# Kernel tuning notes

Hardware: AMD Instinct MI355X
Metric: run time of the kernel (lower is better)

The kernel has to match this reference:

```python
import jax, jax.numpy as jnp
import numpy as np

N_NODES = 100000
IN_CH = 256
OUT_CH = 128
HID = 2 * OUT_CH  # 256
N_EDGES = 1600000


def gcn_conv(x, src, dst, W, b, num_nodes):
    """PyG GCNConv: add self-loops, symmetric deg^-1/2 normalization,
    linear transform, scatter-add aggregation, plus bias."""
    h = x @ W  # [N, F_out]
    loop = jnp.arange(num_nodes, dtype=src.dtype)
    src_f = jnp.concatenate([src, loop])
    dst_f = jnp.concatenate([dst, loop])
    ones = jnp.ones(src_f.shape[0], dtype=h.dtype)
    deg = jax.ops.segment_sum(ones, dst_f, num_segments=num_nodes)
    dis = jnp.where(deg > 0, jax.lax.rsqrt(deg), 0.0)
    norm = dis[src_f] * dis[dst_f]  # [E+N]
    msg = h[src_f] * norm[:, None]  # [E+N, F_out]
    out = jax.ops.segment_sum(msg, dst_f, num_segments=num_nodes)
    return out + b


def setup_inputs() -> dict:
    key = jax.random.key(0)
    ks = jax.random.split(key, 8)
    x = jax.random.normal(ks[0], (N_NODES, IN_CH), dtype=jnp.float32)
    edge_index = jax.random.randint(ks[1], (2, N_EDGES), 0, N_NODES, dtype=jnp.int64 if jax.config.jax_enable_x64 else jnp.int32)
    s1 = 1.0 / np.sqrt(IN_CH)
    s2 = 1.0 / np.sqrt(HID)
    W1 = jax.random.uniform(ks[2], (IN_CH, HID), jnp.float32, -s1, s1)
    b1 = jnp.zeros((HID,), jnp.float32)
    W_mu = jax.random.uniform(ks[3], (HID, OUT_CH), jnp.float32, -s2, s2)
    b_mu = jnp.zeros((OUT_CH,), jnp.float32)
    W_lv = jax.random.uniform(ks[4], (HID, OUT_CH), jnp.float32, -s2, s2)
    b_lv = jnp.zeros((OUT_CH,), jnp.float32)
    return {"x": x, "edge_index": edge_index, "W1": W1, "b1": b1,
            "W_mu": W_mu, "b_mu": b_mu, "W_lv": W_lv, "b_lv": b_lv}


def reference(x, edge_index, W1, b1, W_mu, b_mu, W_lv, b_lv):
    src, dst = edge_index[0], edge_index[1]
    h = jax.nn.relu(gcn_conv(x, src, dst, W1, b1, N_NODES))
    mu = gcn_conv(h, src, dst, W_mu, b_mu, N_NODES)
    logvar = gcn_conv(h, src, dst, W_lv, b_lv, N_NODES)
    return (mu, logvar)
```

## Files before the change

kernel.cpp:

```cpp
#include <hip/hip_runtime.h>
#include <hip/hip_fp16.h>

#define N_NODES 100000
#define E_EDGES 1600000
#define F 256
#define LV_OFF 12800000
#define NBUK 782
#define EPB 8192
#define NBLK_BIN 196

typedef _Float16 half8 __attribute__((ext_vector_type(8)));
typedef _Float16 f16x4 __attribute__((ext_vector_type(4)));
typedef float    f32x4 __attribute__((ext_vector_type(4)));

__global__ void k_zero(int* __restrict__ p, int n) {
    int i = blockIdx.x * 256 + threadIdx.x;
    if (i < n) p[i] = 0;
}

__global__ __launch_bounds__(256) void k_wprep_binA(
    const float* __restrict__ W1, const float* __restrict__ Wmu, const float* __restrict__ Wlv,
    _Float16* __restrict__ Wt1, _Float16* __restrict__ Wtc,
    const int* __restrict__ dst, int* __restrict__ gcnt, int* __restrict__ cbase)
{
    __shared__ int h[NBUK];
    int bid = blockIdx.x, tid = threadIdx.x;
    if (bid < 256) {
        int idx = bid * 256 + tid;
        int n = idx >> 8, k = idx & 255;
        Wt1[n * 256 + k] = (_Float16)W1[k * 256 + n];
        float wc = (n < 128) ? Wmu[k * 128 + n] : Wlv[k * 128 + (n - 128)];
        Wtc[n * 256 + k] = (_Float16)wc;
        return;
    }
    int blk = bid - 256;
    for (int b = tid; b < NBUK; b += 256) h[b] = 0;
    __syncthreads();
    int e0 = blk * EPB, e1 = min(e0 + EPB, E_EDGES);
    for (int e = e0 + tid; e < e1; e += 256) atomicAdd(&h[dst[e] >> 7], 1);
    __syncthreads();
    for (int b = tid; b < NBUK; b += 256) {
        int c = h[b];
        cbase[blk * NBUK + b] = c ? atomicAdd(&gcnt[b], c) : 0;
    }
}

__global__ __launch_bounds__(1024) void k_scan782(const int* __restrict__ gcnt,
                                                  int* __restrict__ gbase) {
    __shared__ int sd[1024];
    int tid = threadIdx.x;
    int v = (tid < NBUK) ? gcnt[tid] : 0;
    sd[tid] = v;
    __syncthreads();
    for (int off = 1; off < 1024; off <<= 1) {
        int t = (tid >= off) ? sd[tid - off] : 0;
        __syncthreads();
        sd[tid] += t;
        __syncthreads();
    }
    if (tid < NBUK) gbase[tid] = sd[tid] - v;
    if (tid == NBUK - 1) gbase[NBUK] = sd[tid];
}

__global__ __launch_bounds__(256) void k_binD(const unsigned long long* __restrict__ ebuf,
                                              const int* __restrict__ gbase,
                                              int* __restrict__ csr_src, int* __restrict__ row_off,
                                              float* __restrict__ dis) {
    __shared__ int dh[128], dsc[128], dcur[128];
    int b = blockIdx.x, tid = threadIdx.x;
    if (tid < 128) dh[tid] = 0;
    __syncthreads();
    int s0 = gbase[b], s1 = gbase[b + 1];
    for (int i = s0 + tid; i < s1; i += 256)
        atomicAdd(&dh[(int)(ebuf[i] >> 32) & 127], 1);
    __syncthreads();
    if (tid < 128) dsc[tid] = dh[tid];
    __syncthreads();
    for (int off = 1; off < 128; off <<= 1) {
        int t = 0;
        if (tid < 128 && tid >= off) t = dsc[tid - off];
        __syncthreads();
        if (tid < 128) dsc[tid] += t;
        __syncthreads();
    }
    if (tid < 128) {
        int ex = dsc[tid] - dh[tid];
        dcur[tid] = ex;
        int node = b * 128 + tid;
        if (node < N_NODES) {
            row_off[node] = s0 + ex;
            dis[node] = rsqrtf((float)dh[tid] + 1.0f);
        }
    }
    if (b == 0 && tid == 128) row_off[N_NODES] = E_EDGES;
    __syncthreads();
    for (int i = s0 + tid; i < s1; i += 256) {
        unsigned long long ed = ebuf[i];
        int dl = (int)(ed >> 32) & 127;
        int lr = atomicAdd(&dcur[dl], 1);
        csr_src[s0 + lr] = (int)(ed & 0xFFFFFFFFull);
    }
}

template <typename TA>
__device__ __forceinline__ void gemm_tile(
    const TA* __restrict__ A, const _Float16* __restrict__ Bt,
    _Float16* __restrict__ G, int M, int m0, int tid, _Float16* Ah, _Float16* Bh)
{
    const int wave = tid >> 6, lane = tid & 63;
    const int wm   = wave & 1, wn = wave >> 1;
    const int lrow = lane & 15, kgrp = lane >> 4;

    f32x4 acc[4][8];
#pragma unroll
    for (int i = 0; i < 4; i++)
#pragma unroll
        for (int j = 0; j < 8; j++) acc[i][j] = (f32x4){0.f, 0.f, 0.f, 0.f};

    for (int kt = 0; kt < 256; kt += 64) {
        if constexpr (sizeof(TA) == 4) {
            const int sr = tid >> 4, kq = tid & 15;
#pragma unroll
            for (int p = 0; p < 8; ++p) {
                int row = p * 16 + sr;
                int gm = m0 + row; if (gm >= M) gm = M - 1;
                float4 v = *reinterpret_cast<const float4*>((const float*)A + (size_t)gm * F + kt + kq * 4);
                f16x4 h4;
                h4[0] = (_Float16)v.x; h4[1] = (_Float16)v.y;
                h4[2] = (_Float16)v.z; h4[3] = (_Float16)v.w;
                *reinterpret_cast<f16x4*>(&Ah[row * 64 + ((kq * 4) ^ ((row & 7) << 3))]) = h4;
            }
        } else {
#pragma unroll
            for (int p = 0; p < 4; ++p) {
                int u = p * 256 + tid;
                int row = u >> 3, slot = u & 7;
                int gm = m0 + row; if (gm >= M) gm = M - 1;
                half8 v = *reinterpret_cast<const half8*>((const _Float16*)A + (size_t)gm * F + kt + slot * 8);
                *reinterpret_cast<half8*>(&Ah[row * 64 + ((slot * 8) ^ ((row & 7) << 3))]) = v;
            }
        }
#pragma unroll
        for (int p = 0; p < 8; ++p) {
            int u = p * 256 + tid;
            int n = u >> 3, slot = u & 7;
            half8 v = *reinterpret_cast<const half8*>(Bt + (size_t)n * F + kt + slot * 8);
            *reinterpret_cast<half8*>(&Bh[n * 64 + ((slot * 8) ^ ((n & 7) << 3))]) = v;
        }
        __syncthreads();
#pragma unroll
        for (int ks = 0; ks < 2; ++ks) {
            int kk = ks * 32 + kgrp * 8;
            half8 ah[4], bh[8];
#pragma unroll
            for (int i = 0; i < 4; ++i) {
                int row = wm * 64 + i * 16 + lrow;
                ah[i] = *reinterpret_cast<const half8*>(&Ah[row * 64 + (kk ^ ((row & 7) << 3))]);
            }
#pragma unroll
            for (int j = 0; j < 8; ++j) {
                int col = wn * 128 + j * 16 + lrow;
                bh[j] = *reinterpret_cast<const half8*>(&Bh[col * 64 + (kk ^ ((col & 7) << 3))]);
            }
#pragma unroll
            for (int i = 0; i < 4; ++i)
#pragma unroll
                for (int j = 0; j < 8; ++j)
                    acc[i][j] = __builtin_amdgcn_mfma_f32_16x16x32_f16(ah[i], bh[j], acc[i][j], 0, 0, 0);
        }
        __syncthreads();
    }

#pragma unroll
    for (int i = 0; i < 4; ++i) {
#pragma unroll
        for (int r = 0; r < 4; ++r) {
            int m = m0 + wm * 64 + i * 16 + kgrp * 4 + r;
            if (m >= M) continue;
#pragma unroll
            for (int j = 0; j < 8; ++j) {
                int n = wn * 128 + j * 16 + lrow;
                G[(size_t)m * F + n] = (_Float16)(acc[i][j][r]);
            }
        }
    }
}

__global__ __launch_bounds__(256, 2) void k_gemm_binC(
    const float* __restrict__ A, const _Float16* __restrict__ Bt,
    _Float16* __restrict__ G, int M,
    const int* __restrict__ src, const int* __restrict__ dst,
    const int* __restrict__ gbase, const int* __restrict__ cbase,
    unsigned long long* __restrict__ ebuf)
{
    __shared__ _Float16 smem[128 * 64 + 256 * 64];
    int bid = blockIdx.x, tid = threadIdx.x;
    int r5 = bid % 5;
    if (r5 < 4) {
        int gid = (bid / 5) * 4 + r5;
        if (gid < 782)
            gemm_tile<float>(A, Bt, G, M, gid * 128, tid, smem, smem + 128 * 64);
        return;
    }
    int* h2 = (int*)smem;
    int* bs = h2 + NBUK;
    int blk = bid / 5;
    for (int b = tid; b < NBUK; b += 256) {
        h2[b] = 0;
        bs[b] = gbase[b] + cbase[blk * NBUK + b];
    }
    __syncthreads();
    int e0 = blk * EPB, e1 = min(e0 + EPB, E_EDGES);
    for (int e = e0 + tid; e < e1; e += 256) {
        int d = dst[e];
        int b = d >> 7;
        int lr = atomicAdd(&h2[b], 1);
        ebuf[bs[b] + lr] = ((unsigned long long)(unsigned)d << 32) | (unsigned)src[e];
    }
}

__global__ __launch_bounds__(256, 2) void k_gemm_f16(
    const _Float16* __restrict__ A, const _Float16* __restrict__ Bt,
    _Float16* __restrict__ G, int M)
{
    __shared__ _Float16 smem[128 * 64 + 256 * 64];
    gemm_tile<_Float16>(A, Bt, G, M, blockIdx.x * 128, threadIdx.x, smem, smem + 128 * 64);
}

template <int RELU>
__device__ __forceinline__ void aggregate_body(
    const _Float16* __restrict__ g, const int* __restrict__ row_off,
    const int* __restrict__ csr_src, const float* __restrict__ dis,
    const float* __restrict__ bmu, const float* __restrict__ blv,
    _Float16* __restrict__ hout, float* __restrict__ out)
{
    int d = blockIdx.x * 4 + (threadIdx.x >> 6);
    int lane = threadIdx.x & 63;
    int hf = lane >> 5, lp = lane & 31;
    const half8* g8 = reinterpret_cast<const half8*>(g);
    float dd = dis[d];
    float a0[8] = {0,0,0,0,0,0,0,0}, a1[8] = {0,0,0,0,0,0,0,0};
    float a2[8] = {0,0,0,0,0,0,0,0}, a3[8] = {0,0,0,0,0,0,0,0};
    if (hf == 0) {
        half8 sv = g8[(size_t)d * 32 + lp];
#pragma unroll
        for (int k = 0; k < 8; k++) a0[k] = dd * (float)sv[k];
    }
    int j0 = row_off[d], j1 = row_off[d + 1];
    int j = j0 + hf;
    for (; j + 14 < j1; j += 16) {
        int s[8]; half8 v[8]; float dv[8];
#pragma unroll
        for (int p = 0; p < 8; ++p) s[p] = csr_src[j + 2 * p];
#pragma unroll
        for (int p = 0; p < 8; ++p) v[p] = g8[(size_t)s[p] * 32 + lp];
#pragma unroll
        for (int p = 0; p < 8; ++p) dv[p] = dis[s[p]];
#pragma unroll
        for (int k = 0; k < 8; k++) {
            a0[k] += dv[0] * (float)v[0][k]; a1[k] += dv[1] * (float)v[1][k];
            a2[k] += dv[2] * (float)v[2][k]; a3[k] += dv[3] * (float)v[3][k];
            a0[k] += dv[4] * (float)v[4][k]; a1[k] += dv[5] * (float)v[5][k];
            a2[k] += dv[6] * (float)v[6][k]; a3[k] += dv[7] * (float)v[7][k];
        }
    }
    for (; j + 2 < j1; j += 4) {
        int sA = csr_src[j], sB = csr_src[j + 2];
        half8 vA = g8[(size_t)sA * 32 + lp];
        half8 vB = g8[(size_t)sB * 32 + lp];
        float dA = dis[sA], dB = dis[sB];
#pragma unroll
        for (int k = 0; k < 8; k++) { a0[k] += dA * (float)vA[k]; a1[k] += dB * (float)vB[k]; }
    }
    if (j < j1) {
        int sA = csr_src[j];
        half8 vA = g8[(size_t)sA * 32 + lp];
        float dA = dis[sA];
#pragma unroll
        for (int k = 0; k < 8; k++) a0[k] += dA * (float)vA[k];
    }
#pragma unroll
    for (int k = 0; k < 8; k++) {
        a0[k] += a1[k] + a2[k] + a3[k];
        a0[k] += __shfl_xor(a0[k], 32);
    }
    if (RELU) {
        int c = lp * 8 + hf * 4;
        float4 bb = *reinterpret_cast<const float4*>(bmu + c);
        f16x4 o;
        o[0] = (_Float16)fmaxf(fmaf(dd, a0[hf * 4 + 0], bb.x), 0.0f);
        o[1] = (_Float16)fmaxf(fmaf(dd, a0[hf * 4 + 1], bb.y), 0.0f);
        o[2] = (_Float16)fmaxf(fmaf(dd, a0[hf * 4 + 2], bb.z), 0.0f);
        o[3] = (_Float16)fmaxf(fmaf(dd, a0[hf * 4 + 3], bb.w), 0.0f);
        *reinterpret_cast<f16x4*>(hout + (size_t)d * F + c) = o;
    } else {
        int ch = lp * 8 + hf * 4;
        float va = a0[hf * 4 + 0], vb = a0[hf * 4 + 1], vc = a0[hf * 4 + 2], vd = a0[hf * 4 + 3];
        if (ch < 128) {
            float4 bb = *reinterpret_cast<const float4*>(bmu + ch);
            float4 o = make_float4(fmaf(dd, va, bb.x), fmaf(dd, vb, bb.y),
                                   fmaf(dd, vc, bb.z), fmaf(dd, vd, bb.w));
            *reinterpret_cast<float4*>(out + (size_t)d * 128 + ch) = o;
        } else {
            int c2 = ch - 128;
            float4 bb = *reinterpret_cast<const float4*>(blv + c2);
            float4 o = make_float4(fmaf(dd, va, bb.x), fmaf(dd, vb, bb.y),
                                   fmaf(dd, vc, bb.z), fmaf(dd, vd, bb.w));
            *reinterpret_cast<float4*>(out + LV_OFF + (size_t)d * 128 + c2) = o;
        }
    }
}

__global__ __launch_bounds__(256) void k_aggregate_relu(
    const _Float16* __restrict__ g, const int* __restrict__ row_off,
    const int* __restrict__ csr_src, const float* __restrict__ dis,
    const float* __restrict__ b, _Float16* __restrict__ h)
{
    aggregate_body<1>(g, row_off, csr_src, dis, b, nullptr, h, nullptr);
}

__global__ __launch_bounds__(256) void k_aggregate_out(
    const _Float16* __restrict__ g, const int* __restrict__ row_off,
    const int* __restrict__ csr_src, const float* __restrict__ dis,
    const float* __restrict__ bmu, const float* __restrict__ blv,
    float* __restrict__ out)
{
    aggregate_body<0>(g, row_off, csr_src, dis, bmu, blv, nullptr, out);
}

extern "C" void kernel_launch(void* const* d_in, const int* in_sizes, int n_in,
                              void* d_out, int out_size, void* d_ws, size_t ws_size,
                              hipStream_t stream) {
    const float* x   = (const float*)d_in[0];
    const int*   ei  = (const int*)d_in[1];
    const int*   src = ei;
    const int*   dst = ei + E_EDGES;
    const float* W1  = (const float*)d_in[2];
    const float* b1  = (const float*)d_in[3];
    const float* Wmu = (const float*)d_in[4];
    const float* bmu = (const float*)d_in[5];
    const float* Wlv = (const float*)d_in[6];
    const float* blv = (const float*)d_in[7];
    float* out = (float*)d_out;

    char* ws = (char*)d_ws;
    size_t o = 0;
    auto carve = [&](size_t bytes) -> char* {
        char* p = ws + o;
        o = (o + bytes + 1023) & ~(size_t)1023;
        return p;
    };
    float*    dis     = (float*)   carve(400000);
    int*      row_off = (int*)     carve(400004);
    int*      gcnt    = (int*)     carve(NBUK * 4);
    int*      gbase   = (int*)     carve((NBUK + 1) * 4);
    int*      cbase   = (int*)     carve((size_t)NBLK_BIN * NBUK * 4);
    _Float16* Wt1     = (_Float16*)carve(131072);
    _Float16* Wtc     = (_Float16*)carve(131072);
    int*      csr_src = (int*)     carve((size_t)E_EDGES * 4);
    unsigned long long* ebuf = (unsigned long long*)carve((size_t)E_EDGES * 8);
    _Float16* g       = (_Float16*)carve((size_t)N_NODES * F * 2);
    (void)ws_size;

    _Float16* h16 = (_Float16*)(out + LV_OFF);

    k_zero      <<<(NBUK + 255) / 256, 256, 0, stream>>>(gcnt, NBUK);
    k_wprep_binA<<<256 + NBLK_BIN, 256, 0, stream>>>(W1, Wmu, Wlv, Wt1, Wtc, dst, gcnt, cbase);
    k_scan782   <<<1, 1024, 0, stream>>>(gcnt, gbase);
    k_gemm_binC <<<980, 256, 0, stream>>>(x, Wt1, g, N_NODES, src, dst, gbase, cbase, ebuf);
    k_binD      <<<NBUK, 256, 0, stream>>>(ebuf, gbase, csr_src, row_off, dis);

    k_aggregate_relu<<<N_NODES / 4, 256, 0, stream>>>(g, row_off, csr_src, dis, b1, h16);

    k_gemm_f16<<<782, 256, 0, stream>>>(h16, Wtc, g, N_NODES);
    k_aggregate_out<<<N_NODES / 4, 256, 0, stream>>>(g, row_off, csr_src, dis, bmu, blv, out);
}
```

Baseline: 422.7 us.

## Fold source-side degree scaling into GEMM epilogue and streamline aggregation

Per-node degree counts are now computed early with global atomics, so dis is available before the GEMMs. Each GEMM output row is pre-scaled by dis[src] in its epilogue. This removes the per-edge dis[s] gathers and multiplies from both aggregation kernels, whose inner loop becomes packed fp16-to-fp32 mix-FMAs (v_fma_mix_f32). The change also adds nontemporal loads for GEMM inputs and nontemporal output stores, and reduces the aggregation accumulators from four to two. The cost is an extra 1.6M-edge atomic count pass and an fp16 rounding of the pre-scaled values.

```diff
diff --git a/kernel.cpp b/kernel.cpp
--- a/kernel.cpp
+++ b/kernel.cpp
@@ -8,20 +8,38 @@
 #define NBUK 782
 #define EPB 8192
 #define NBLK_BIN 196
+#define CNT_BLKS 6250
 
 typedef _Float16 half8 __attribute__((ext_vector_type(8)));
 typedef _Float16 f16x4 __attribute__((ext_vector_type(4)));
 typedef float    f32x4 __attribute__((ext_vector_type(4)));
-
-__global__ void k_zero(int* __restrict__ p, int n) {
+typedef unsigned u32x4 __attribute__((ext_vector_type(4)));
+
+__device__ __forceinline__ void fmix2(float& lo, float& hi, unsigned v) {
+    asm("v_fma_mix_f32 %0, %2, 1.0, %0 op_sel_hi:[1,0,0]\n\t"
+        "v_fma_mix_f32 %1, %2, 1.0, %1 op_sel:[1,0,0] op_sel_hi:[1,0,0]"
+        : "+v"(lo), "+v"(hi) : "v"(v));
+}
+
+__device__ __forceinline__ void acc_row(float* a, half8 v) {
+    u32x4 u = __builtin_bit_cast(u32x4, v);
+    fmix2(a[0], a[1], u[0]);
+    fmix2(a[2], a[3], u[1]);
+    fmix2(a[4], a[5], u[2]);
+    fmix2(a[6], a[7], u[3]);
+}
+
+__global__ void k_zero2(int* __restrict__ cnt, int* __restrict__ gcnt) {
     int i = blockIdx.x * 256 + threadIdx.x;
-    if (i < n) p[i] = 0;
-}
-
-__global__ __launch_bounds__(256) void k_wprep_binA(
+    if (i < N_NODES) cnt[i] = 0;
+    if (i < NBUK) gcnt[i] = 0;
+}
+
+__global__ __launch_bounds__(256) void k_prep(
     const float* __restrict__ W1, const float* __restrict__ Wmu, const float* __restrict__ Wlv,
     _Float16* __restrict__ Wt1, _Float16* __restrict__ Wtc,
-    const int* __restrict__ dst, int* __restrict__ gcnt, int* __restrict__ cbase)
+    const int* __restrict__ dst, int* __restrict__ gcnt, int* __restrict__ cbase,
+    int* __restrict__ cnt)
 {
     __shared__ int h[NBUK];
     int bid = blockIdx.x, tid = threadIdx.x;
@@ -33,6 +51,11 @@
         Wtc[n * 256 + k] = (_Float16)wc;
         return;
     }
+    if (bid >= 256 + NBLK_BIN) {
+        int e = (bid - 256 - NBLK_BIN) * 256 + tid;
+        if (e < E_EDGES) atomicAdd(&cnt[dst[e]], 1);
+        return;
+    }
     int blk = bid - 256;
     for (int b = tid; b < NBUK; b += 256) h[b] = 0;
     __syncthreads();
@@ -45,10 +68,17 @@
     }
 }
 
-__global__ __launch_bounds__(1024) void k_scan782(const int* __restrict__ gcnt,
-                                                  int* __restrict__ gbase) {
+__global__ __launch_bounds__(1024) void k_scan_dis(const int* __restrict__ gcnt,
+                                                   int* __restrict__ gbase,
+                                                   const int* __restrict__ cnt,
+                                                   float* __restrict__ dis) {
+    int tid = threadIdx.x;
+    if (blockIdx.x != 0) {
+        int i = (blockIdx.x - 1) * 1024 + tid;
+        if (i < N_NODES) dis[i] = rsqrtf((float)cnt[i] + 1.0f);
+        return;
+    }
     __shared__ int sd[1024];
-    int tid = threadIdx.x;
     int v = (tid < NBUK) ? gcnt[tid] : 0;
     sd[tid] = v;
     __syncthreads();
@@ -64,8 +94,7 @@
 
 __global__ __launch_bounds__(256) void k_binD(const unsigned long long* __restrict__ ebuf,
                                               const int* __restrict__ gbase,
-                                              int* __restrict__ csr_src, int* __restrict__ row_off,
-                                              float* __restrict__ dis) {
+                                              int* __restrict__ csr_src, int* __restrict__ row_off) {
     __shared__ int dh[128], dsc[128], dcur[128];
     int b = blockIdx.x, tid = threadIdx.x;
     if (tid < 128) dh[tid] = 0;
@@ -87,10 +116,7 @@
         int ex = dsc[tid] - dh[tid];
         dcur[tid] = ex;
         int node = b * 128 + tid;
-        if (node < N_NODES) {
-            row_off[node] = s0 + ex;
-            dis[node] = rsqrtf((float)dh[tid] + 1.0f);
-        }
+        if (node < N_NODES) row_off[node] = s0 + ex;
     }
     if (b == 0 && tid == 128) row_off[N_NODES] = E_EDGES;
     __syncthreads();
@@ -105,7 +131,8 @@
 template <typename TA>
 __device__ __forceinline__ void gemm_tile(
     const TA* __restrict__ A, const _Float16* __restrict__ Bt,
-    _Float16* __restrict__ G, int M, int m0, int tid, _Float16* Ah, _Float16* Bh)
+    const float* __restrict__ dis, _Float16* __restrict__ G, int M,
+    int m0, int tid, _Float16* Ah, _Float16* Bh)
 {
     const int wave = tid >> 6, lane = tid & 63;
     const int wm   = wave & 1, wn = wave >> 1;
@@ -124,10 +151,11 @@
             for (int p = 0; p < 8; ++p) {
                 int row = p * 16 + sr;
                 int gm = m0 + row; if (gm >= M) gm = M - 1;
-                float4 v = *reinterpret_cast<const float4*>((const float*)A + (size_t)gm * F + kt + kq * 4);
+                f32x4 v = __builtin_nontemporal_load(
+                    reinterpret_cast<const f32x4*>((const float*)A + (size_t)gm * F + kt + kq * 4));
                 f16x4 h4;
-                h4[0] = (_Float16)v.x; h4[1] = (_Float16)v.y;
-                h4[2] = (_Float16)v.z; h4[3] = (_Float16)v.w;
+                h4[0] = (_Float16)v[0]; h4[1] = (_Float16)v[1];
+                h4[2] = (_Float16)v[2]; h4[3] = (_Float16)v[3];
                 *reinterpret_cast<f16x4*>(&Ah[row * 64 + ((kq * 4) ^ ((row & 7) << 3))]) = h4;
             }
         } else {
@@ -136,7 +164,8 @@
                 int u = p * 256 + tid;
                 int row = u >> 3, slot = u & 7;
                 int gm = m0 + row; if (gm >= M) gm = M - 1;
-                half8 v = *reinterpret_cast<const half8*>((const _Float16*)A + (size_t)gm * F + kt + slot * 8);
+                half8 v = __builtin_nontemporal_load(
+                    reinterpret_cast<const half8*>((const _Float16*)A + (size_t)gm * F + kt + slot * 8));
                 *reinterpret_cast<half8*>(&Ah[row * 64 + ((slot * 8) ^ ((row & 7) << 3))]) = v;
             }
         }
@@ -177,10 +206,11 @@
         for (int r = 0; r < 4; ++r) {
             int m = m0 + wm * 64 + i * 16 + kgrp * 4 + r;
             if (m >= M) continue;
+            float dv = dis[m];
 #pragma unroll
             for (int j = 0; j < 8; ++j) {
                 int n = wn * 128 + j * 16 + lrow;
-                G[(size_t)m * F + n] = (_Float16)(acc[i][j][r]);
+                G[(size_t)m * F + n] = (_Float16)(acc[i][j][r] * dv);
             }
         }
     }
@@ -188,7 +218,7 @@
 
 __global__ __launch_bounds__(256, 2) void k_gemm_binC(
     const float* __restrict__ A, const _Float16* __restrict__ Bt,
-    _Float16* __restrict__ G, int M,
+    const float* __restrict__ dis, _Float16* __restrict__ G, int M,
     const int* __restrict__ src, const int* __restrict__ dst,
     const int* __restrict__ gbase, const int* __restrict__ cbase,
     unsigned long long* __restrict__ ebuf)
@@ -199,7 +229,7 @@
     if (r5 < 4) {
         int gid = (bid / 5) * 4 + r5;
         if (gid < 782)
-            gemm_tile<float>(A, Bt, G, M, gid * 128, tid, smem, smem + 128 * 64);
+            gemm_tile<float>(A, Bt, dis, G, M, gid * 128, tid, smem, smem + 128 * 64);
         return;
     }
     int* h2 = (int*)smem;
@@ -221,10 +251,10 @@
 
 __global__ __launch_bounds__(256, 2) void k_gemm_f16(
     const _Float16* __restrict__ A, const _Float16* __restrict__ Bt,
-    _Float16* __restrict__ G, int M)
+    const float* __restrict__ dis, _Float16* __restrict__ G, int M)
 {
     __shared__ _Float16 smem[128 * 64 + 256 * 64];
-    gemm_tile<_Float16>(A, Bt, G, M, blockIdx.x * 128, threadIdx.x, smem, smem + 128 * 64);
+    gemm_tile<_Float16>(A, Bt, dis, G, M, blockIdx.x * 128, threadIdx.x, smem, smem + 128 * 64);
 }
 
 template <int RELU>
@@ -238,52 +268,44 @@
     int lane = threadIdx.x & 63;
     int hf = lane >> 5, lp = lane & 31;
     const half8* g8 = reinterpret_cast<const half8*>(g);
-    float dd = dis[d];
     float a0[8] = {0,0,0,0,0,0,0,0}, a1[8] = {0,0,0,0,0,0,0,0};
-    float a2[8] = {0,0,0,0,0,0,0,0}, a3[8] = {0,0,0,0,0,0,0,0};
     if (hf == 0) {
         half8 sv = g8[(size_t)d * 32 + lp];
 #pragma unroll
-        for (int k = 0; k < 8; k++) a0[k] = dd * (float)sv[k];
+        for (int k = 0; k < 8; k++) a0[k] = (float)sv[k];
     }
     int j0 = row_off[d], j1 = row_off[d + 1];
     int j = j0 + hf;
-    for (; j + 14 < j1; j += 16) {
-        int s[8]; half8 v[8]; float dv[8];
-#pragma unroll
-        for (int p = 0; p < 8; ++p) s[p] = csr_src[j + 2 * p];
-#pragma unroll
-        for (int p = 0; p < 8; ++p) v[p] = g8[(size_t)s[p] * 32 + lp];
-#pragma unroll
-        for (int p = 0; p < 8; ++p) dv[p] = dis[s[p]];
-#pragma unroll
-        for (int k = 0; k < 8; k++) {
-            a0[k] += dv[0] * (float)v[0][k]; a1[k] += dv[1] * (float)v[1][k];
-            a2[k] += dv[2] * (float)v[2][k]; a3[k] += dv[3] * (float)v[3][k];
-            a0[k] += dv[4] * (float)v[4][k]; a1[k] += dv[5] * (float)v[5][k];
-            a2[k] += dv[6] * (float)v[6][k]; a3[k] += dv[7] * (float)v[7][k];
-        }
+    for (; j + 10 < j1; j += 12) {
+        int s0 = csr_src[j],     s1 = csr_src[j + 2], s2 = csr_src[j + 4];
+        int s3 = csr_src[j + 6], s4 = csr_src[j + 8], s5 = csr_src[j + 10];
+        half8 v0 = g8[(size_t)s0 * 32 + lp];
+        half8 v1 = g8[(size_t)s1 * 32 + lp];
+        half8 v2 = g8[(size_t)s2 * 32 + lp];
+        half8 v3 = g8[(size_t)s3 * 32 + lp];
+        half8 v4 = g8[(size_t)s4 * 32 + lp];
+        half8 v5 = g8[(size_t)s5 * 32 + lp];
+        acc_row(a0, v0); acc_row(a1, v1);
+        acc_row(a0, v2); acc_row(a1, v3);
+        acc_row(a0, v4); acc_row(a1, v5);
     }
     for (; j + 2 < j1; j += 4) {
         int sA = csr_src[j], sB = csr_src[j + 2];
         half8 vA = g8[(size_t)sA * 32 + lp];
         half8 vB = g8[(size_t)sB * 32 + lp];
-        float dA = dis[sA], dB = dis[sB];
-#pragma unroll
-        for (int k = 0; k < 8; k++) { a0[k] += dA * (float)vA[k]; a1[k] += dB * (float)vB[k]; }
+        acc_row(a0, vA); acc_row(a1, vB);
     }
     if (j < j1) {
         int sA = csr_src[j];
         half8 vA = g8[(size_t)sA * 32 + lp];
-        float dA = dis[sA];
-#pragma unroll
-        for (int k = 0; k < 8; k++) a0[k] += dA * (float)vA[k];
+        acc_row(a0, vA);
     }
 #pragma unroll
     for (int k = 0; k < 8; k++) {
-        a0[k] += a1[k] + a2[k] + a3[k];
+        a0[k] += a1[k];
         a0[k] += __shfl_xor(a0[k], 32);
     }
+    float dd = dis[d];
     if (RELU) {
         int c = lp * 8 + hf * 4;
         float4 bb = *reinterpret_cast<const float4*>(bmu + c);
@@ -298,15 +320,15 @@
         float va = a0[hf * 4 + 0], vb = a0[hf * 4 + 1], vc = a0[hf * 4 + 2], vd = a0[hf * 4 + 3];
         if (ch < 128) {
             float4 bb = *reinterpret_cast<const float4*>(bmu + ch);
-            float4 o = make_float4(fmaf(dd, va, bb.x), fmaf(dd, vb, bb.y),
-                                   fmaf(dd, vc, bb.z), fmaf(dd, vd, bb.w));
-            *reinterpret_cast<float4*>(out + (size_t)d * 128 + ch) = o;
+            f32x4 o = {fmaf(dd, va, bb.x), fmaf(dd, vb, bb.y),
+                       fmaf(dd, vc, bb.z), fmaf(dd, vd, bb.w)};
+            __builtin_nontemporal_store(o, reinterpret_cast<f32x4*>(out + (size_t)d * 128 + ch));
         } else {
             int c2 = ch - 128;
             float4 bb = *reinterpret_cast<const float4*>(blv + c2);
-            float4 o = make_float4(fmaf(dd, va, bb.x), fmaf(dd, vb, bb.y),
-                                   fmaf(dd, vc, bb.z), fmaf(dd, vd, bb.w));
-            *reinterpret_cast<float4*>(out + LV_OFF + (size_t)d * 128 + c2) = o;
+            f32x4 o = {fmaf(dd, va, bb.x), fmaf(dd, vb, bb.y),
+                       fmaf(dd, vc, bb.z), fmaf(dd, vd, bb.w)};
+            __builtin_nontemporal_store(o, reinterpret_cast<f32x4*>(out + LV_OFF + (size_t)d * 128 + c2));
         }
     }
 }
@@ -351,6 +373,7 @@
         return p;
     };
     float*    dis     = (float*)   carve(400000);
+    int*      cnt     = (int*)     carve(400000);
     int*      row_off = (int*)     carve(400004);
     int*      gcnt    = (int*)     carve(NBUK * 4);
     int*      gbase   = (int*)     carve((NBUK + 1) * 4);
@@ -364,14 +387,15 @@
 
     _Float16* h16 = (_Float16*)(out + LV_OFF);
 
-    k_zero      <<<(NBUK + 255) / 256, 256, 0, stream>>>(gcnt, NBUK);
-    k_wprep_binA<<<256 + NBLK_BIN, 256, 0, stream>>>(W1, Wmu, Wlv, Wt1, Wtc, dst, gcnt, cbase);
-    k_scan782   <<<1, 1024, 0, stream>>>(gcnt, gbase);
-    k_gemm_binC <<<980, 256, 0, stream>>>(x, Wt1, g, N_NODES, src, dst, gbase, cbase, ebuf);
-    k_binD      <<<NBUK, 256, 0, stream>>>(ebuf, gbase, csr_src, row_off, dis);
+    k_zero2   <<<(N_NODES + 255) / 256, 256, 0, stream>>>(cnt, gcnt);
+    k_prep    <<<256 + NBLK_BIN + CNT_BLKS, 256, 0, stream>>>(W1, Wmu, Wlv, Wt1, Wtc,
+                                                              dst, gcnt, cbase, cnt);
+    k_scan_dis<<<99, 1024, 0, stream>>>(gcnt, gbase, cnt, dis);
+    k_gemm_binC<<<980, 256, 0, stream>>>(x, Wt1, dis, g, N_NODES, src, dst, gbase, cbase, ebuf);
+    k_binD     <<<NBUK, 256, 0, stream>>>(ebuf, gbase, csr_src, row_off);
 
     k_aggregate_relu<<<N_NODES / 4, 256, 0, stream>>>(g, row_off, csr_src, dis, b1, h16);
 
-    k_gemm_f16<<<782, 256, 0, stream>>>(h16, Wtc, g, N_NODES);
+    k_gemm_f16<<<782, 256, 0, stream>>>(h16, Wtc, dis, g, N_NODES);
     k_aggregate_out<<<N_NODES / 4, 256, 0, stream>>>(g, row_off, csr_src, dis, bmu, blv, out);
 }
```

New measurement: 427.4 us. Within noise of the previous version (+1.1%).
